# Kernel tuning notes

Measured on AMD Instinct MI355X. Metric: run time of the kernel, lower is better.

The kernel has to match this reference:

```python
import jax, jax.numpy as jnp
import numpy as np

N, F, C = 4096, 512, 512
NUM_HOPS, TOP_K, MASK_RATIO = 3, 8, 0.5
EPS = 1e-12


def setup_inputs() -> dict:
    key = jax.random.key(0)
    ks = jax.random.split(key, 8)
    return {
        "x": jax.random.normal(ks[0], (N, F), dtype=jnp.float32),
        "adj": jax.random.uniform(ks[1], (NUM_HOPS, N, N), dtype=jnp.float32),
        "rand_mask": jax.random.uniform(ks[2], (NUM_HOPS, N, N), dtype=jnp.float32),
        "W_in": jax.random.normal(ks[3], (F, C), dtype=jnp.float32) * 0.02,
        "b_in": jnp.zeros((C,), dtype=jnp.float32),
        "W_out": jax.random.normal(ks[4], (C, C), dtype=jnp.float32) * 0.02,
        "b_out": jnp.zeros((C,), dtype=jnp.float32),
        "alpha": jnp.ones((NUM_HOPS,), dtype=jnp.float32),
        "beta": jnp.full((1,), 0.5, dtype=jnp.float32),
    }


def reference(x, adj, rand_mask, W_in, b_in, W_out, b_out, alpha, beta):
    H_low = x @ W_in + b_in  # (N, C)
    # F.normalize(x, dim=-1) @ F.normalize(x.T, dim=0) == x_n @ x_n.T
    xn = x / jnp.maximum(jnp.linalg.norm(x, axis=-1, keepdims=True), EPS)
    sim = xn @ xn.T  # (N, N)
    a = jax.nn.softmax(alpha)
    rows = jnp.arange(N)[:, None]
    H_high = jnp.zeros((N, F), dtype=x.dtype)
    for k in range(NUM_HOPS):
        Akw = a[k] * adj[k] * sim  # (N, N)
        _, idx = jax.lax.top_k(Akw, TOP_K)  # (N, TOP_K)
        topk_mask = jnp.zeros_like(Akw).at[rows, idx].set(1.0)
        retain = (rand_mask[k] < MASK_RATIO).astype(Akw.dtype)
        final_mask = ((topk_mask + retain) > 0).astype(Akw.dtype)
        Hk = (Akw * final_mask) @ x  # (N, F)
        H_high = H_high + a[k] * Hk
    b = beta[0]
    H = jax.nn.relu(b * H_low + (1.0 - b) * H_high)
    # dropout in eval mode (identity)
    out = H @ W_out + b_out
    return jax.nn.log_softmax(out, axis=-1)
```

## Files before the change

kernel.cpp:

```cpp
#include <hip/hip_runtime.h>
#include <hip/hip_bf16.h>
#include <stdint.h>

#define NROW 4096
#define FDIM 512

typedef short bf16x8 __attribute__((ext_vector_type(8)));
typedef float f32x4 __attribute__((ext_vector_type(4)));
typedef float f4 __attribute__((ext_vector_type(4)));
typedef ushort u16x4 __attribute__((ext_vector_type(4)));

#define NEG_INF (-__builtin_inff())

__device__ inline ushort f2bf(float f) {
    union { float f; uint32_t u; } c{f};
    uint32_t u = c.u;
    uint32_t r = (u + 0x7FFF + ((u >> 16) & 1)) >> 16;
    return (ushort)r;
}
__device__ inline float bf2f(ushort h) {
    union { uint32_t u; float f; } c{((uint32_t)h) << 16};
    return c.f;
}
__device__ inline uint32_t cvt_pk_bf16(float lo, float hi) {
    uint32_t r;
    asm("v_cvt_pk_bf16_f32 %0, %1, %2" : "=v"(r) : "v"(lo), "v"(hi));
    return r;
}
__device__ inline float up0(uint32_t p) {
    union { uint32_t u; float f; } c{p << 16}; return c.f;
}
__device__ inline float up1(uint32_t p) {
    union { uint32_t u; float f; } c{p & 0xFFFF0000u}; return c.f;
}

__device__ inline float waveReduceMax(float v) {
    #pragma unroll
    for (int o = 32; o > 0; o >>= 1) v = fmaxf(v, __shfl_xor(v, o));
    return v;
}
__device__ inline float waveReduceSum(float v) {
    #pragma unroll
    for (int o = 32; o > 0; o >>= 1) v += __shfl_xor(v, o);
    return v;
}

__device__ inline void CE(float& a, float& b) {
    float mx = fmaxf(a, b);
    b = fminf(a, b);
    a = mx;
}
__device__ inline void sort8(float (&l)[8]) {
    CE(l[0],l[1]); CE(l[2],l[3]); CE(l[4],l[5]); CE(l[6],l[7]);
    CE(l[0],l[2]); CE(l[1],l[3]); CE(l[4],l[6]); CE(l[5],l[7]);
    CE(l[1],l[2]); CE(l[5],l[6]);
    CE(l[0],l[4]); CE(l[1],l[5]); CE(l[2],l[6]); CE(l[3],l[7]);
    CE(l[2],l[4]); CE(l[3],l[5]);
    CE(l[1],l[2]); CE(l[3],l[4]); CE(l[5],l[6]);
}
__device__ inline void mergeTop8(float (&a)[8], const float (&b)[8]) {
    float t[8];
    #pragma unroll
    for (int i = 0; i < 8; i++) t[i] = fmaxf(a[i], b[7 - i]);
    CE(t[0],t[4]); CE(t[1],t[5]); CE(t[2],t[6]); CE(t[3],t[7]);
    CE(t[0],t[2]); CE(t[1],t[3]); CE(t[4],t[6]); CE(t[5],t[7]);
    CE(t[0],t[1]); CE(t[2],t[3]); CE(t[4],t[5]); CE(t[6],t[7]);
    #pragma unroll
    for (int i = 0; i < 8; i++) a[i] = t[i];
}

#define GLL16(src, dst)                                                        \
    __builtin_amdgcn_global_load_lds(                                          \
        (const __attribute__((address_space(1))) void*)(src),                  \
        (__attribute__((address_space(3))) void*)(dst), 16, 0, 0)

__global__ __launch_bounds__(64) void coef_k(const float* __restrict__ alpha,
                                             const float* __restrict__ beta,
                                             float* __restrict__ coef) {
    if (threadIdx.x == 0) {
        float a0 = alpha[0], a1 = alpha[1], a2 = alpha[2];
        float m = fmaxf(a0, fmaxf(a1, a2));
        float e0 = expf(a0 - m), e1 = expf(a1 - m), e2 = expf(a2 - m);
        float s = e0 + e1 + e2;
        coef[0] = e0 / s; coef[1] = e1 / s; coef[2] = e2 / s;
        coef[3] = beta[0];
    }
}

__global__ __launch_bounds__(256) void prep_x(const float* __restrict__ x,
                                              ushort* __restrict__ xn,
                                              ushort* __restrict__ xb) {
    int row = blockIdx.x, tid = threadIdx.x;
    int lane = tid & 63, w = tid >> 6;
    const float* xr = x + (size_t)row * FDIM;
    float v0 = xr[tid], v1 = xr[tid + 256];
    float ss = v0 * v0 + v1 * v1;
    ss = waveReduceSum(ss);
    __shared__ float b4[4];
    if (lane == 0) b4[w] = ss;
    __syncthreads();
    float tot = b4[0] + b4[1] + b4[2] + b4[3];
    float inv = 1.f / fmaxf(sqrtf(tot), 1e-12f);
    size_t o = (size_t)row * FDIM + tid;
    xn[o] = f2bf(v0 * inv);  xn[o + 256] = f2bf(v1 * inv);
    xb[o] = f2bf(v0);        xb[o + 256] = f2bf(v1);
}

__global__ __launch_bounds__(256) void transpose_xb(const ushort* __restrict__ in,
                                                    ushort* __restrict__ out) {
    __shared__ ushort t[64][65];
    int lx = threadIdx.x & 63, ly = threadIdx.x >> 6;
    int c0 = blockIdx.x * 64, r0 = blockIdx.y * 64;
    #pragma unroll
    for (int i = 0; i < 16; i++)
        t[ly + 4 * i][lx] = in[(size_t)(r0 + ly + 4 * i) * FDIM + c0 + lx];
    __syncthreads();
    #pragma unroll
    for (int i = 0; i < 16; i++)
        out[(size_t)(c0 + ly + 4 * i) * NROW + r0 + lx] = t[lx][ly + 4 * i];
}

__global__ __launch_bounds__(256) void convT_w(const float* __restrict__ Wf,
                                               ushort* __restrict__ WT) {
    __shared__ ushort t[64][65];
    int lx = threadIdx.x & 63, ly = threadIdx.x >> 6;
    int c0 = blockIdx.x * 64, r0 = blockIdx.y * 64;
    #pragma unroll
    for (int i = 0; i < 16; i++)
        t[ly + 4 * i][lx] = f2bf(Wf[(size_t)(r0 + ly + 4 * i) * 512 + c0 + lx]);
    __syncthreads();
    #pragma unroll
    for (int i = 0; i < 16; i++)
        WT[(size_t)(c0 + ly + 4 * i) * 512 + r0 + lx] = t[lx][ly + 4 * i];
}

template <int EPI>
__global__ __launch_bounds__(256) void gemm_abT(
    const ushort* __restrict__ A, int lda,
    const ushort* __restrict__ B, int ldb,
    int Kdim, int ldc,
    float* __restrict__ Cf, ushort* __restrict__ Cb,
    const float* __restrict__ bias) {
    constexpr int BK = 64;
    constexpr int NT = 128 * BK;
    constexpr int CPR = BK / 8;
    constexpr int PASSES = (128 * CPR) / 256;
    __shared__ __align__(16) ushort smem[2 * NT];
    ushort* As = smem;
    ushort* Bs = smem + NT;

    if constexpr (EPI == 3) {
        A += (size_t)blockIdx.z * 1024;
        B += (size_t)blockIdx.z * 1024;
        Cf += (size_t)blockIdx.z * ((size_t)NROW * 512);
    }

    const int tid = threadIdx.x;
    const int lane = tid & 63, w = tid >> 6;
    const int wr = w >> 1, wc = w & 1;
    const int m0 = blockIdx.y * 128;
    const int n0 = blockIdx.x * 128;

    f32x4 acc[4][4];
    #pragma unroll
    for (int mi = 0; mi < 4; mi++)
        #pragma unroll
        for (int ni = 0; ni < 4; ni++)
            #pragma unroll
            for (int r = 0; r < 4; r++) acc[mi][ni][r] = 0.f;

    for (int k0 = 0; k0 < Kdim; k0 += BK) {
        #pragma unroll
        for (int p = 0; p < PASSES; ++p) {
            int chunk = p * 256 + tid;
            int row = chunk / CPR;
            int kc = chunk % CPR;
            const ushort* asrc = A + (size_t)(m0 + row) * lda + k0 + kc * 8;
            const ushort* bsrc = B + (size_t)(n0 + row) * ldb + k0 + kc * 8;
            ushort* abase = As + (size_t)(p * 256 + w * 64) * 8;
            ushort* bbase = Bs + (size_t)(p * 256 + w * 64) * 8;
            GLL16(asrc, abase);
            GLL16(bsrc, bbase);
        }
        __syncthreads();
        #pragma unroll
        for (int kf = 0; kf < BK / 32; ++kf) {
            const int ko = kf * 32 + (lane >> 4) * 8;
            bf16x8 av[4], bv[4];
            #pragma unroll
            for (int mi = 0; mi < 4; mi++)
                av[mi] = *(const bf16x8*)&As[(wr * 64 + mi * 16 + (lane & 15)) * BK + ko];
            #pragma unroll
            for (int ni = 0; ni < 4; ni++)
                bv[ni] = *(const bf16x8*)&Bs[(wc * 64 + ni * 16 + (lane & 15)) * BK + ko];
            #pragma unroll
            for (int mi = 0; mi < 4; mi++)
                #pragma unroll
                for (int ni = 0; ni < 4; ni++)
                    acc[mi][ni] = __builtin_amdgcn_mfma_f32_16x16x32_bf16(
                        av[mi], bv[ni], acc[mi][ni], 0, 0, 0);
        }
        __syncthreads();
    }

    #pragma unroll
    for (int mi = 0; mi < 4; mi++) {
        #pragma unroll
        for (int ni = 0; ni < 4; ni++) {
            int col = n0 + wc * 64 + ni * 16 + (lane & 15);
            #pragma unroll
            for (int r = 0; r < 4; r++) {
                int rowg = m0 + wr * 64 + mi * 16 + (lane >> 4) * 4 + r;
                size_t off = (size_t)rowg * ldc + col;
                float v = acc[mi][ni][r];
                if constexpr (EPI == 1) {
                    Cf[off] = v + bias[col];
                } else if constexpr (EPI == 3) {
                    Cf[off] = v;
                } else {
                    Cb[off] = f2bf(v);
                }
            }
        }
    }
}

__global__ __launch_bounds__(256) void topk_build_M(
    const ushort* __restrict__ simb, const float* __restrict__ adj,
    const float* __restrict__ rmask, const float* __restrict__ coef,
    ushort* __restrict__ Mout) {
    const int tid = threadIdx.x;
    const int lane = tid & 63;
    const int w = tid >> 6;
    const int row = blockIdx.x;
    __shared__ float wl[3][4][8];

    const int cbase = w * 1024 + lane * 4;

    const ushort* srow = simb + (size_t)row * NROW + cbase;
    uint2 svp[4];
    #pragma unroll
    for (int q = 0; q < 4; q++)
        svp[q] = *(const uint2*)(srow + q * 256);

    float macc[4][4];
    #pragma unroll
    for (int q = 0; q < 4; q++)
        #pragma unroll
        for (int c = 0; c < 4; c++) macc[q][c] = 0.f;

    for (int k = 0; k < 3; ++k) {
        const float* arow = adj + ((size_t)k * NROW + row) * NROW + cbase;
        const float* rrow = rmask + ((size_t)k * NROW + row) * NROW + cbase;

        f4 rv[4], a[4];
        #pragma unroll
        for (int q = 0; q < 4; q++) rv[q] = *(const f4*)(rrow + q * 256);
        #pragma unroll
        for (int q = 0; q < 4; q++) a[q] = *(const f4*)(arow + q * 256);

        uint32_t rbits = 0;
        #pragma unroll
        for (int q = 0; q < 4; q++) {
            rbits |= (rv[q].x < 0.5f ? 1u : 0u) << (q * 4 + 0);
            rbits |= (rv[q].y < 0.5f ? 1u : 0u) << (q * 4 + 1);
            rbits |= (rv[q].z < 0.5f ? 1u : 0u) << (q * 4 + 2);
            rbits |= (rv[q].w < 0.5f ? 1u : 0u) << (q * 4 + 3);
        }

        uint2 avp[4];
        #pragma unroll
        for (int q = 0; q < 4; q++) {
            avp[q].x = cvt_pk_bf16(a[q].x, a[q].y);
            avp[q].y = cvt_pk_bf16(a[q].z, a[q].w);
        }

        float lo8[8], hi8[8];
        #pragma unroll
        for (int qq = 0; qq < 2; qq++) {
            lo8[qq * 4 + 0] = up0(avp[qq].x) * up0(svp[qq].x);
            lo8[qq * 4 + 1] = up1(avp[qq].x) * up1(svp[qq].x);
            lo8[qq * 4 + 2] = up0(avp[qq].y) * up0(svp[qq].y);
            lo8[qq * 4 + 3] = up1(avp[qq].y) * up1(svp[qq].y);
        }
        #pragma unroll
        for (int qq = 0; qq < 2; qq++) {
            const int q = 2 + qq;
            hi8[qq * 4 + 0] = up0(avp[q].x) * up0(svp[q].x);
            hi8[qq * 4 + 1] = up1(avp[q].x) * up1(svp[q].x);
            hi8[qq * 4 + 2] = up0(avp[q].y) * up0(svp[q].y);
            hi8[qq * 4 + 3] = up1(avp[q].y) * up1(svp[q].y);
        }
        sort8(lo8);
        sort8(hi8);
        mergeTop8(lo8, hi8);

        #pragma unroll
        for (int lvl = 0; lvl < 6; lvl++) {
            float b[8];
            #pragma unroll
            for (int i = 0; i < 8; i++) b[i] = __shfl_xor(lo8[i], 1 << lvl);
            mergeTop8(lo8, b);
        }

        if (lane < 8) wl[k][w][lane] = lo8[lane];
        __syncthreads();
        #pragma unroll
        for (int ww = 0; ww < 4; ww++) {
            if (ww != w) {
                float b[8];
                #pragma unroll
                for (int i = 0; i < 8; i++) b[i] = wl[k][ww][i];
                mergeTop8(lo8, b);
            }
        }
        const float thr = lo8[7];

        const float ak = coef[k];
        const float aksq = ak * ak;
        #pragma unroll
        for (int q = 0; q < 4; q++) {
            float av0 = up0(avp[q].x), av1 = up1(avp[q].x);
            float av2 = up0(avp[q].y), av3 = up1(avp[q].y);
            float s0 = up0(svp[q].x), s1 = up1(svp[q].x);
            float s2 = up0(svp[q].y), s3 = up1(svp[q].y);
            bool m0 = ((rbits >> (q * 4 + 0)) & 1) || (av0 * s0 >= thr);
            bool m1 = ((rbits >> (q * 4 + 1)) & 1) || (av1 * s1 >= thr);
            bool m2 = ((rbits >> (q * 4 + 2)) & 1) || (av2 * s2 >= thr);
            bool m3 = ((rbits >> (q * 4 + 3)) & 1) || (av3 * s3 >= thr);
            macc[q][0] += m0 ? aksq * av0 : 0.f;
            macc[q][1] += m1 ? aksq * av1 : 0.f;
            macc[q][2] += m2 ? aksq * av2 : 0.f;
            macc[q][3] += m3 ? aksq * av3 : 0.f;
        }
    }

    ushort* mrow = Mout + (size_t)row * NROW + cbase;
    #pragma unroll
    for (int q = 0; q < 4; q++) {
        u16x4 o;
        o[0] = f2bf(up0(svp[q].x) * macc[q][0]);
        o[1] = f2bf(up1(svp[q].x) * macc[q][1]);
        o[2] = f2bf(up0(svp[q].y) * macc[q][2]);
        o[3] = f2bf(up1(svp[q].y) * macc[q][3]);
        *(u16x4*)(mrow + q * 256) = o;
    }
}

__global__ __launch_bounds__(256) void reduce_relu(
    const float* __restrict__ parts, const float* __restrict__ hlow,
    const float* __restrict__ coef, ushort* __restrict__ Hb) {
    const size_t i = (size_t)blockIdx.x * 256 + threadIdx.x;
    const f4* p4 = (const f4*)parts;
    f4 s = p4[i];
    #pragma unroll
    for (int z = 1; z < 4; z++) s += p4[(size_t)z * 524288 + i];
    f4 hl = ((const f4*)hlow)[i];
    float cb = coef[3];
    u16x4 o;
    #pragma unroll
    for (int c = 0; c < 4; c++) {
        float h = cb * hl[c] + (1.f - cb) * s[c];
        o[c] = f2bf(fmaxf(h, 0.f));
    }
    *((u16x4*)Hb + i) = o;
}

__global__ __launch_bounds__(256) void logsoftmax_k(const float* __restrict__ L,
                                                    float* __restrict__ out) {
    int row = blockIdx.x, tid = threadIdx.x;
    int lane = tid & 63, w = tid >> 6;
    const float* lr = L + (size_t)row * 512;
    float v0 = lr[tid], v1 = lr[tid + 256];
    __shared__ float bm[4], bs[4];
    float m = fmaxf(v0, v1);
    m = waveReduceMax(m);
    if (lane == 0) bm[w] = m;
    __syncthreads();
    float M = fmaxf(fmaxf(bm[0], bm[1]), fmaxf(bm[2], bm[3]));
    float s = expf(v0 - M) + expf(v1 - M);
    s = waveReduceSum(s);
    if (lane == 0) bs[w] = s;
    __syncthreads();
    float S = bs[0] + bs[1] + bs[2] + bs[3];
    float lse = M + logf(S);
    float* orow = out + (size_t)row * 512;
    orow[tid] = v0 - lse;
    orow[tid + 256] = v1 - lse;
}

extern "C" void kernel_launch(void* const* d_in, const int* in_sizes, int n_in,
                              void* d_out, int out_size, void* d_ws, size_t ws_size,
                              hipStream_t stream) {
    const float* x     = (const float*)d_in[0];
    const float* adj   = (const float*)d_in[1];
    const float* rmask = (const float*)d_in[2];
    const float* W_in  = (const float*)d_in[3];
    const float* b_in  = (const float*)d_in[4];
    const float* W_out = (const float*)d_in[5];
    const float* b_out = (const float*)d_in[6];
    const float* alpha = (const float*)d_in[7];
    const float* beta  = (const float*)d_in[8];
    float* out = (float*)d_out;

    const size_t MB = 1024 * 1024;
    char* wsb = (char*)d_ws;
    ushort* simb   = (ushort*)wsb;
    float*  parts  = (float*)wsb;
    float*  logits = (float*)wsb;
    ushort* Mb     = (ushort*)(wsb + 32 * MB);
    ushort* xn     = (ushort*)(wsb + 64 * MB);
    ushort* xb     = (ushort*)(wsb + 68 * MB);
    ushort* xbT    = (ushort*)(wsb + 72 * MB);
    ushort* WinT   = (ushort*)(wsb + 76 * MB);
    ushort* WoutT  = (ushort*)(wsb + 76 * MB + 512 * 1024);
    float*  Hlow   = (float*)(wsb + 77 * MB);
    ushort* Hb     = (ushort*)(wsb + 85 * MB);
    float*  coef   = (float*)(wsb + 89 * MB);

    coef_k<<<1, 64, 0, stream>>>(alpha, beta, coef);
    prep_x<<<NROW, 256, 0, stream>>>(x, xn, xb);
    transpose_xb<<<dim3(8, 64), 256, 0, stream>>>(xb, xbT);
    convT_w<<<dim3(8, 8), 256, 0, stream>>>(W_in, WinT);
    convT_w<<<dim3(8, 8), 256, 0, stream>>>(W_out, WoutT);

    gemm_abT<4><<<dim3(32, 32), 256, 0, stream>>>(
        xn, FDIM, xn, FDIM, FDIM, NROW, nullptr, simb, nullptr);

    topk_build_M<<<NROW, 256, 0, stream>>>(simb, adj, rmask, coef, Mb);

    gemm_abT<1><<<dim3(4, 32), 256, 0, stream>>>(
        xb, FDIM, WinT, FDIM, FDIM, 512, Hlow, nullptr, b_in);

    gemm_abT<3><<<dim3(4, 32, 4), 256, 0, stream>>>(
        Mb, NROW, xbT, NROW, 1024, 512, parts, nullptr, nullptr);

    reduce_relu<<<2048, 256, 0, stream>>>(parts, Hlow, coef, Hb);

    gemm_abT<1><<<dim3(4, 32), 256, 0, stream>>>(
        Hb, 512, WoutT, 512, 512, 512, logits, nullptr, b_out);

    logsoftmax_k<<<NROW, 256, 0, stream>>>(logits, out);
}
```

Baseline: 217.6 us.

## Assign one wavefront per row in top-k mask build, merge weight transpose launches

The top-k mask kernel now gives each row to a single wavefront instead of a whole block. This removes the shared-memory exchange and __syncthreads between waves. Each wave makes two passes: first it streams adj and sim to find the per-hop thresholds, then it re-reads adj, rand_mask and sim chunk by chunk to build M. The cost is a second read of adj from memory, or from cache if it still fits, in exchange for fewer syncs and lower register pressure. The two weight transpose kernels are also merged into a single launch.

```diff
diff --git a/kernel.cpp b/kernel.cpp
--- a/kernel.cpp
+++ b/kernel.cpp
@@ -120,8 +120,12 @@
         out[(size_t)(c0 + ly + 4 * i) * NROW + r0 + lx] = t[lx][ly + 4 * i];
 }
 
-__global__ __launch_bounds__(256) void convT_w(const float* __restrict__ Wf,
-                                               ushort* __restrict__ WT) {
+__global__ __launch_bounds__(256) void convT_w2(const float* __restrict__ W0,
+                                                ushort* __restrict__ T0,
+                                                const float* __restrict__ W1,
+                                                ushort* __restrict__ T1) {
+    const float* Wf = blockIdx.z ? W1 : W0;
+    ushort* WT = blockIdx.z ? T1 : T0;
     __shared__ ushort t[64][65];
     int lx = threadIdx.x & 63, ly = threadIdx.x >> 6;
     int c0 = blockIdx.x * 64, r0 = blockIdx.y * 64;
@@ -225,6 +229,68 @@
     }
 }
 
+__device__ __attribute__((always_inline)) inline void chunk_top8(
+    const f4 (&a)[4], const uint2 (&sp)[4], float (&t)[8]) {
+    float u[8];
+    #pragma unroll
+    for (int qq = 0; qq < 2; qq++) {
+        uint32_t p0 = cvt_pk_bf16(a[qq].x, a[qq].y);
+        uint32_t p1 = cvt_pk_bf16(a[qq].z, a[qq].w);
+        t[qq * 4 + 0] = up0(p0) * up0(sp[qq].x);
+        t[qq * 4 + 1] = up1(p0) * up1(sp[qq].x);
+        t[qq * 4 + 2] = up0(p1) * up0(sp[qq].y);
+        t[qq * 4 + 3] = up1(p1) * up1(sp[qq].y);
+    }
+    #pragma unroll
+    for (int qq = 0; qq < 2; qq++) {
+        const int q = 2 + qq;
+        uint32_t p0 = cvt_pk_bf16(a[q].x, a[q].y);
+        uint32_t p1 = cvt_pk_bf16(a[q].z, a[q].w);
+        u[qq * 4 + 0] = up0(p0) * up0(sp[q].x);
+        u[qq * 4 + 1] = up1(p0) * up1(sp[q].x);
+        u[qq * 4 + 2] = up0(p1) * up0(sp[q].y);
+        u[qq * 4 + 3] = up1(p1) * up1(sp[q].y);
+    }
+    sort8(t);
+    sort8(u);
+    mergeTop8(t, u);
+}
+
+template <int K>
+__device__ __attribute__((always_inline)) inline float hop_threshold(
+    const float* __restrict__ arow, const ushort* __restrict__ srow,
+    int loff) {
+    const size_t hopstride = (size_t)NROW * NROW;
+    float l[8];
+    #pragma unroll
+    for (int c = 0; c < 4; ++c) {
+        f4 a[4];
+        uint2 sp[4];
+        #pragma unroll
+        for (int q = 0; q < 4; q++)
+            a[q] = *(const f4*)(arow + K * hopstride + c * 1024 + q * 256 + loff);
+        #pragma unroll
+        for (int q = 0; q < 4; q++)
+            sp[q] = *(const uint2*)(srow + c * 1024 + q * 256 + loff);
+        float t[8];
+        chunk_top8(a, sp, t);
+        if (c == 0) {
+            #pragma unroll
+            for (int i = 0; i < 8; i++) l[i] = t[i];
+        } else {
+            mergeTop8(l, t);
+        }
+    }
+    #pragma unroll
+    for (int lvl = 0; lvl < 6; lvl++) {
+        float b[8];
+        #pragma unroll
+        for (int i = 0; i < 8; i++) b[i] = __shfl_xor(l[i], 1 << lvl);
+        mergeTop8(l, b);
+    }
+    return l[7];
+}
+
 __global__ __launch_bounds__(256) void topk_build_M(
     const ushort* __restrict__ simb, const float* __restrict__ adj,
     const float* __restrict__ rmask, const float* __restrict__ coef,
@@ -232,118 +298,74 @@
     const int tid = threadIdx.x;
     const int lane = tid & 63;
     const int w = tid >> 6;
-    const int row = blockIdx.x;
-    __shared__ float wl[3][4][8];
-
-    const int cbase = w * 1024 + lane * 4;
-
-    const ushort* srow = simb + (size_t)row * NROW + cbase;
-    uint2 svp[4];
-    #pragma unroll
-    for (int q = 0; q < 4; q++)
-        svp[q] = *(const uint2*)(srow + q * 256);
-
-    float macc[4][4];
-    #pragma unroll
-    for (int q = 0; q < 4; q++)
-        #pragma unroll
-        for (int c = 0; c < 4; c++) macc[q][c] = 0.f;
-
-    for (int k = 0; k < 3; ++k) {
-        const float* arow = adj + ((size_t)k * NROW + row) * NROW + cbase;
-        const float* rrow = rmask + ((size_t)k * NROW + row) * NROW + cbase;
-
-        f4 rv[4], a[4];
-        #pragma unroll
-        for (int q = 0; q < 4; q++) rv[q] = *(const f4*)(rrow + q * 256);
-        #pragma unroll
-        for (int q = 0; q < 4; q++) a[q] = *(const f4*)(arow + q * 256);
-
-        uint32_t rbits = 0;
+    const int row = blockIdx.x * 4 + w;
+    const int loff = lane * 4;
+    const size_t hopstride = (size_t)NROW * NROW;
+
+    const ushort* srow = simb + (size_t)row * NROW;
+    const float* arow = adj + (size_t)row * NROW;
+    const float* rrow = rmask + (size_t)row * NROW;
+
+    const float thr0 = hop_threshold<0>(arow, srow, loff);
+    const float thr1 = hop_threshold<1>(arow, srow, loff);
+    const float thr2 = hop_threshold<2>(arow, srow, loff);
+
+    const float c0 = coef[0], c1 = coef[1], c2 = coef[2];
+
+    #pragma unroll 1
+    for (int c = 0; c < 4; ++c) {
+        uint2 sp[4];
+        #pragma unroll
+        for (int q = 0; q < 4; q++)
+            sp[q] = *(const uint2*)(srow + c * 1024 + q * 256 + loff);
+
+        float macc[4][4];
+        #pragma unroll
+        for (int q = 0; q < 4; q++)
+            #pragma unroll
+            for (int e = 0; e < 4; e++) macc[q][e] = 0.f;
+
+        #pragma unroll
+        for (int k = 0; k < 3; ++k) {
+            const float ak = (k == 0) ? c0 : (k == 1) ? c1 : c2;
+            const float thr = (k == 0) ? thr0 : (k == 1) ? thr1 : thr2;
+            const float aksq = ak * ak;
+            f4 a[4], rv[4];
+            #pragma unroll
+            for (int q = 0; q < 4; q++)
+                rv[q] = *(const f4*)(rrow + k * hopstride + c * 1024 + q * 256 + loff);
+            #pragma unroll
+            for (int q = 0; q < 4; q++)
+                a[q] = *(const f4*)(arow + k * hopstride + c * 1024 + q * 256 + loff);
+            #pragma unroll
+            for (int q = 0; q < 4; q++) {
+                uint32_t p0 = cvt_pk_bf16(a[q].x, a[q].y);
+                uint32_t p1 = cvt_pk_bf16(a[q].z, a[q].w);
+                float av0 = up0(p0), av1 = up1(p0);
+                float av2 = up0(p1), av3 = up1(p1);
+                float s0 = up0(sp[q].x), s1 = up1(sp[q].x);
+                float s2 = up0(sp[q].y), s3 = up1(sp[q].y);
+                bool m0 = (rv[q].x < 0.5f) || (av0 * s0 >= thr);
+                bool m1 = (rv[q].y < 0.5f) || (av1 * s1 >= thr);
+                bool m2 = (rv[q].z < 0.5f) || (av2 * s2 >= thr);
+                bool m3 = (rv[q].w < 0.5f) || (av3 * s3 >= thr);
+                macc[q][0] += m0 ? aksq * av0 : 0.f;
+                macc[q][1] += m1 ? aksq * av1 : 0.f;
+                macc[q][2] += m2 ? aksq * av2 : 0.f;
+                macc[q][3] += m3 ? aksq * av3 : 0.f;
+            }
+        }
+
+        ushort* mrow = Mout + (size_t)row * NROW + c * 1024 + loff;
         #pragma unroll
         for (int q = 0; q < 4; q++) {
-            rbits |= (rv[q].x < 0.5f ? 1u : 0u) << (q * 4 + 0);
-            rbits |= (rv[q].y < 0.5f ? 1u : 0u) << (q * 4 + 1);
-            rbits |= (rv[q].z < 0.5f ? 1u : 0u) << (q * 4 + 2);
-            rbits |= (rv[q].w < 0.5f ? 1u : 0u) << (q * 4 + 3);
-        }
-
-        uint2 avp[4];
-        #pragma unroll
-        for (int q = 0; q < 4; q++) {
-            avp[q].x = cvt_pk_bf16(a[q].x, a[q].y);
-            avp[q].y = cvt_pk_bf16(a[q].z, a[q].w);
-        }
-
-        float lo8[8], hi8[8];
-        #pragma unroll
-        for (int qq = 0; qq < 2; qq++) {
-            lo8[qq * 4 + 0] = up0(avp[qq].x) * up0(svp[qq].x);
-            lo8[qq * 4 + 1] = up1(avp[qq].x) * up1(svp[qq].x);
-            lo8[qq * 4 + 2] = up0(avp[qq].y) * up0(svp[qq].y);
-            lo8[qq * 4 + 3] = up1(avp[qq].y) * up1(svp[qq].y);
-        }
-        #pragma unroll
-        for (int qq = 0; qq < 2; qq++) {
-            const int q = 2 + qq;
-            hi8[qq * 4 + 0] = up0(avp[q].x) * up0(svp[q].x);
-            hi8[qq * 4 + 1] = up1(avp[q].x) * up1(svp[q].x);
-            hi8[qq * 4 + 2] = up0(avp[q].y) * up0(svp[q].y);
-            hi8[qq * 4 + 3] = up1(avp[q].y) * up1(svp[q].y);
-        }
-        sort8(lo8);
-        sort8(hi8);
-        mergeTop8(lo8, hi8);
-
-        #pragma unroll
-        for (int lvl = 0; lvl < 6; lvl++) {
-            float b[8];
-            #pragma unroll
-            for (int i = 0; i < 8; i++) b[i] = __shfl_xor(lo8[i], 1 << lvl);
-            mergeTop8(lo8, b);
-        }
-
-        if (lane < 8) wl[k][w][lane] = lo8[lane];
-        __syncthreads();
-        #pragma unroll
-        for (int ww = 0; ww < 4; ww++) {
-            if (ww != w) {
-                float b[8];
-                #pragma unroll
-                for (int i = 0; i < 8; i++) b[i] = wl[k][ww][i];
-                mergeTop8(lo8, b);
-            }
-        }
-        const float thr = lo8[7];
-
-        const float ak = coef[k];
-        const float aksq = ak * ak;
-        #pragma unroll
-        for (int q = 0; q < 4; q++) {
-            float av0 = up0(avp[q].x), av1 = up1(avp[q].x);
-            float av2 = up0(avp[q].y), av3 = up1(avp[q].y);
-            float s0 = up0(svp[q].x), s1 = up1(svp[q].x);
-            float s2 = up0(svp[q].y), s3 = up1(svp[q].y);
-            bool m0 = ((rbits >> (q * 4 + 0)) & 1) || (av0 * s0 >= thr);
-            bool m1 = ((rbits >> (q * 4 + 1)) & 1) || (av1 * s1 >= thr);
-            bool m2 = ((rbits >> (q * 4 + 2)) & 1) || (av2 * s2 >= thr);
-            bool m3 = ((rbits >> (q * 4 + 3)) & 1) || (av3 * s3 >= thr);
-            macc[q][0] += m0 ? aksq * av0 : 0.f;
-            macc[q][1] += m1 ? aksq * av1 : 0.f;
-            macc[q][2] += m2 ? aksq * av2 : 0.f;
-            macc[q][3] += m3 ? aksq * av3 : 0.f;
-        }
-    }
-
-    ushort* mrow = Mout + (size_t)row * NROW + cbase;
-    #pragma unroll
-    for (int q = 0; q < 4; q++) {
-        u16x4 o;
-        o[0] = f2bf(up0(svp[q].x) * macc[q][0]);
-        o[1] = f2bf(up1(svp[q].x) * macc[q][1]);
-        o[2] = f2bf(up0(svp[q].y) * macc[q][2]);
-        o[3] = f2bf(up1(svp[q].y) * macc[q][3]);
-        *(u16x4*)(mrow + q * 256) = o;
+            u16x4 o;
+            o[0] = f2bf(up0(sp[q].x) * macc[q][0]);
+            o[1] = f2bf(up1(sp[q].x) * macc[q][1]);
+            o[2] = f2bf(up0(sp[q].y) * macc[q][2]);
+            o[3] = f2bf(up1(sp[q].y) * macc[q][3]);
+            *(u16x4*)(mrow + q * 256) = o;
+        }
     }
 }
 
@@ -421,13 +443,12 @@
     coef_k<<<1, 64, 0, stream>>>(alpha, beta, coef);
     prep_x<<<NROW, 256, 0, stream>>>(x, xn, xb);
     transpose_xb<<<dim3(8, 64), 256, 0, stream>>>(xb, xbT);
-    convT_w<<<dim3(8, 8), 256, 0, stream>>>(W_in, WinT);
-    convT_w<<<dim3(8, 8), 256, 0, stream>>>(W_out, WoutT);
+    convT_w2<<<dim3(8, 8, 2), 256, 0, stream>>>(W_in, WinT, W_out, WoutT);
 
     gemm_abT<4><<<dim3(32, 32), 256, 0, stream>>>(
         xn, FDIM, xn, FDIM, FDIM, NROW, nullptr, simb, nullptr);
 
-    topk_build_M<<<NROW, 256, 0, stream>>>(simb, adj, rmask, coef, Mb);
+    topk_build_M<<<NROW / 4, 256, 0, stream>>>(simb, adj, rmask, coef, Mb);
 
     gemm_abT<1><<<dim3(4, 32), 256, 0, stream>>>(
         xb, FDIM, WinT, FDIM, FDIM, 512, Hlow, nullptr, b_in);
```

Result: slower. 242.2 us (+11.3%).

## Exploit symmetry of similarity GEMM and fuse preprocessing kernels

Applied to the files above, without the earlier changes.

Replaces the full 32x32-tile xn·xnᵀ GEMM with a triangular launch of 528 tiles that computes only upper-triangle blocks and writes the transposed copy through shared memory. The separate prep, transpose and weight-conversion kernels are merged into one launch, and the x transpose now converts straight from the fp32 input. The top-k kernel's hop loop is kept rolled and gains a barrier. This roughly halves the similarity GEMM work and cuts launches, at the cost of strided transposed stores and a larger shared-memory tile.

```diff
diff --git a/kernel.cpp b/kernel.cpp
--- a/kernel.cpp
+++ b/kernel.cpp
@@ -17,10 +17,6 @@
     uint32_t u = c.u;
     uint32_t r = (u + 0x7FFF + ((u >> 16) & 1)) >> 16;
     return (ushort)r;
-}
-__device__ inline float bf2f(ushort h) {
-    union { uint32_t u; float f; } c{((uint32_t)h) << 16};
-    return c.f;
 }
 __device__ inline uint32_t cvt_pk_bf16(float lo, float hi) {
     uint32_t r;
@@ -87,51 +83,142 @@
     }
 }
 
-__global__ __launch_bounds__(256) void prep_x(const float* __restrict__ x,
-                                              ushort* __restrict__ xn,
-                                              ushort* __restrict__ xb) {
-    int row = blockIdx.x, tid = threadIdx.x;
-    int lane = tid & 63, w = tid >> 6;
-    const float* xr = x + (size_t)row * FDIM;
-    float v0 = xr[tid], v1 = xr[tid + 256];
-    float ss = v0 * v0 + v1 * v1;
-    ss = waveReduceSum(ss);
+__global__ __launch_bounds__(256) void prep_fused(
+    const float* __restrict__ x, ushort* __restrict__ xn,
+    ushort* __restrict__ xb, ushort* __restrict__ xbT,
+    const float* __restrict__ W_in, ushort* __restrict__ WinT,
+    const float* __restrict__ W_out, ushort* __restrict__ WoutT) {
+    const int b = blockIdx.x;
+    const int tid = threadIdx.x;
     __shared__ float b4[4];
-    if (lane == 0) b4[w] = ss;
-    __syncthreads();
-    float tot = b4[0] + b4[1] + b4[2] + b4[3];
-    float inv = 1.f / fmaxf(sqrtf(tot), 1e-12f);
-    size_t o = (size_t)row * FDIM + tid;
-    xn[o] = f2bf(v0 * inv);  xn[o + 256] = f2bf(v1 * inv);
-    xb[o] = f2bf(v0);        xb[o + 256] = f2bf(v1);
-}
-
-__global__ __launch_bounds__(256) void transpose_xb(const ushort* __restrict__ in,
-                                                    ushort* __restrict__ out) {
     __shared__ ushort t[64][65];
-    int lx = threadIdx.x & 63, ly = threadIdx.x >> 6;
-    int c0 = blockIdx.x * 64, r0 = blockIdx.y * 64;
-    #pragma unroll
-    for (int i = 0; i < 16; i++)
-        t[ly + 4 * i][lx] = in[(size_t)(r0 + ly + 4 * i) * FDIM + c0 + lx];
-    __syncthreads();
-    #pragma unroll
-    for (int i = 0; i < 16; i++)
-        out[(size_t)(c0 + ly + 4 * i) * NROW + r0 + lx] = t[lx][ly + 4 * i];
-}
-
-__global__ __launch_bounds__(256) void convT_w(const float* __restrict__ Wf,
-                                               ushort* __restrict__ WT) {
-    __shared__ ushort t[64][65];
-    int lx = threadIdx.x & 63, ly = threadIdx.x >> 6;
-    int c0 = blockIdx.x * 64, r0 = blockIdx.y * 64;
-    #pragma unroll
-    for (int i = 0; i < 16; i++)
-        t[ly + 4 * i][lx] = f2bf(Wf[(size_t)(r0 + ly + 4 * i) * 512 + c0 + lx]);
-    __syncthreads();
-    #pragma unroll
-    for (int i = 0; i < 16; i++)
-        WT[(size_t)(c0 + ly + 4 * i) * 512 + r0 + lx] = t[lx][ly + 4 * i];
+
+    if (b < 4096) {
+        const int row = b;
+        int lane = tid & 63, w = tid >> 6;
+        const float* xr = x + (size_t)row * FDIM;
+        float v0 = xr[tid], v1 = xr[tid + 256];
+        float ss = v0 * v0 + v1 * v1;
+        ss = waveReduceSum(ss);
+        if (lane == 0) b4[w] = ss;
+        __syncthreads();
+        float tot = b4[0] + b4[1] + b4[2] + b4[3];
+        float inv = 1.f / fmaxf(sqrtf(tot), 1e-12f);
+        size_t o = (size_t)row * FDIM + tid;
+        xn[o] = f2bf(v0 * inv);  xn[o + 256] = f2bf(v1 * inv);
+        xb[o] = f2bf(v0);        xb[o + 256] = f2bf(v1);
+    } else if (b < 4608) {
+        const int tb = b - 4096;
+        const int c0 = (tb & 7) * 64, r0 = (tb >> 3) * 64;
+        int lx = tid & 63, ly = tid >> 6;
+        #pragma unroll
+        for (int i = 0; i < 16; i++)
+            t[ly + 4 * i][lx] = f2bf(x[(size_t)(r0 + ly + 4 * i) * FDIM + c0 + lx]);
+        __syncthreads();
+        #pragma unroll
+        for (int i = 0; i < 16; i++)
+            xbT[(size_t)(c0 + ly + 4 * i) * NROW + r0 + lx] = t[lx][ly + 4 * i];
+    } else {
+        const int cb = b - 4608;
+        const float* Wf = (cb >> 6) ? W_out : W_in;
+        ushort* WT = (cb >> 6) ? WoutT : WinT;
+        const int idx = cb & 63;
+        const int c0 = (idx & 7) * 64, r0 = (idx >> 3) * 64;
+        int lx = tid & 63, ly = tid >> 6;
+        #pragma unroll
+        for (int i = 0; i < 16; i++)
+            t[ly + 4 * i][lx] = f2bf(Wf[(size_t)(r0 + ly + 4 * i) * 512 + c0 + lx]);
+        __syncthreads();
+        #pragma unroll
+        for (int i = 0; i < 16; i++)
+            WT[(size_t)(c0 + ly + 4 * i) * 512 + r0 + lx] = t[lx][ly + 4 * i];
+    }
+}
+
+__global__ __launch_bounds__(256) void gemm_sym(
+    const ushort* __restrict__ A, ushort* __restrict__ C) {
+    constexpr int BK = 64;
+    constexpr int NT = 128 * BK;
+    __shared__ __align__(16) ushort smem[128 * 130];
+    ushort* As = smem;
+    ushort* Bs = smem + NT;
+
+    int bi = 0, rem = blockIdx.x;
+    while (rem >= 32 - bi) { rem -= 32 - bi; bi++; }
+    const int bj = bi + rem;
+    const int m0 = bi * 128, n0 = bj * 128;
+
+    const int tid = threadIdx.x;
+    const int lane = tid & 63, w = tid >> 6;
+    const int wr = w >> 1, wc = w & 1;
+
+    f32x4 acc[4][4];
+    #pragma unroll
+    for (int mi = 0; mi < 4; mi++)
+        #pragma unroll
+        for (int ni = 0; ni < 4; ni++)
+            #pragma unroll
+            for (int r = 0; r < 4; r++) acc[mi][ni][r] = 0.f;
+
+    for (int k0 = 0; k0 < FDIM; k0 += BK) {
+        #pragma unroll
+        for (int p = 0; p < 4; ++p) {
+            int chunk = p * 256 + tid;
+            int row = chunk / 8;
+            int kc = chunk % 8;
+            GLL16(A + (size_t)(m0 + row) * FDIM + k0 + kc * 8,
+                  As + (size_t)(p * 256 + w * 64) * 8);
+            GLL16(A + (size_t)(n0 + row) * FDIM + k0 + kc * 8,
+                  Bs + (size_t)(p * 256 + w * 64) * 8);
+        }
+        __syncthreads();
+        #pragma unroll
+        for (int kf = 0; kf < BK / 32; ++kf) {
+            const int ko = kf * 32 + (lane >> 4) * 8;
+            bf16x8 av[4], bv[4];
+            #pragma unroll
+            for (int mi = 0; mi < 4; mi++)
+                av[mi] = *(const bf16x8*)&As[(wr * 64 + mi * 16 + (lane & 15)) * BK + ko];
+            #pragma unroll
+            for (int ni = 0; ni < 4; ni++)
+                bv[ni] = *(const bf16x8*)&Bs[(wc * 64 + ni * 16 + (lane & 15)) * BK + ko];
+            #pragma unroll
+            for (int mi = 0; mi < 4; mi++)
+                #pragma unroll
+                for (int ni = 0; ni < 4; ni++)
+                    acc[mi][ni] = __builtin_amdgcn_mfma_f32_16x16x32_bf16(
+                        av[mi], bv[ni], acc[mi][ni], 0, 0, 0);
+        }
+        __syncthreads();
+    }
+
+    #pragma unroll
+    for (int mi = 0; mi < 4; mi++) {
+        #pragma unroll
+        for (int ni = 0; ni < 4; ni++) {
+            int lcol = wc * 64 + ni * 16 + (lane & 15);
+            #pragma unroll
+            for (int r = 0; r < 4; r++) {
+                int lrow = wr * 64 + mi * 16 + (lane >> 4) * 4 + r;
+                ushort hv = f2bf(acc[mi][ni][r]);
+                C[(size_t)(m0 + lrow) * NROW + n0 + lcol] = hv;
+                smem[lrow * 130 + lcol] = hv;
+            }
+        }
+    }
+
+    if (bi != bj) {
+        __syncthreads();
+        const int wv = w;
+        #pragma unroll 4
+        for (int i = 0; i < 32; i++) {
+            int r2 = wv * 32 + i;
+            ushort a = smem[(lane * 2) * 130 + r2];
+            ushort bb = smem[(lane * 2 + 1) * 130 + r2];
+            uint32_t pk = (uint32_t)a | ((uint32_t)bb << 16);
+            *(uint32_t*)&C[(size_t)(n0 + r2) * NROW + m0 + lane * 2] = pk;
+        }
+    }
 }
 
 template <int EPI>
@@ -215,10 +302,8 @@
                 float v = acc[mi][ni][r];
                 if constexpr (EPI == 1) {
                     Cf[off] = v + bias[col];
-                } else if constexpr (EPI == 3) {
+                } else {
                     Cf[off] = v;
-                } else {
-                    Cb[off] = f2bf(v);
                 }
             }
         }
@@ -236,8 +321,12 @@
     __shared__ float wl[3][4][8];
 
     const int cbase = w * 1024 + lane * 4;
+    const size_t hopstride = (size_t)NROW * NROW;
 
     const ushort* srow = simb + (size_t)row * NROW + cbase;
+    const float* arow = adj + (size_t)row * NROW + cbase;
+    const float* rrow = rmask + (size_t)row * NROW + cbase;
+
     uint2 svp[4];
     #pragma unroll
     for (int q = 0; q < 4; q++)
@@ -249,15 +338,16 @@
         #pragma unroll
         for (int c = 0; c < 4; c++) macc[q][c] = 0.f;
 
+    #pragma unroll 1
     for (int k = 0; k < 3; ++k) {
-        const float* arow = adj + ((size_t)k * NROW + row) * NROW + cbase;
-        const float* rrow = rmask + ((size_t)k * NROW + row) * NROW + cbase;
+        const float* ar = arow + (size_t)k * hopstride;
+        const float* rr = rrow + (size_t)k * hopstride;
 
         f4 rv[4], a[4];
         #pragma unroll
-        for (int q = 0; q < 4; q++) rv[q] = *(const f4*)(rrow + q * 256);
-        #pragma unroll
-        for (int q = 0; q < 4; q++) a[q] = *(const f4*)(arow + q * 256);
+        for (int q = 0; q < 4; q++) rv[q] = *(const f4*)(rr + q * 256);
+        #pragma unroll
+        for (int q = 0; q < 4; q++) a[q] = *(const f4*)(ar + q * 256);
 
         uint32_t rbits = 0;
         #pragma unroll
@@ -333,6 +423,7 @@
             macc[q][2] += m2 ? aksq * av2 : 0.f;
             macc[q][3] += m3 ? aksq * av3 : 0.f;
         }
+        __syncthreads();
     }
 
     ushort* mrow = Mout + (size_t)row * NROW + cbase;
@@ -419,13 +510,11 @@
     float*  coef   = (float*)(wsb + 89 * MB);
 
     coef_k<<<1, 64, 0, stream>>>(alpha, beta, coef);
-    prep_x<<<NROW, 256, 0, stream>>>(x, xn, xb);
-    transpose_xb<<<dim3(8, 64), 256, 0, stream>>>(xb, xbT);
-    convT_w<<<dim3(8, 8), 256, 0, stream>>>(W_in, WinT);
-    convT_w<<<dim3(8, 8), 256, 0, stream>>>(W_out, WoutT);
-
-    gemm_abT<4><<<dim3(32, 32), 256, 0, stream>>>(
-        xn, FDIM, xn, FDIM, FDIM, NROW, nullptr, simb, nullptr);
+
+    prep_fused<<<4096 + 512 + 128, 256, 0, stream>>>(
+        x, xn, xb, xbT, W_in, WinT, W_out, WoutT);
+
+    gemm_sym<<<528, 256, 0, stream>>>(xn, simb);
 
     topk_build_M<<<NROW, 256, 0, stream>>>(simb, adj, rmask, coef, Mb);
 
```

New measurement: 213.5 us. No clear change (-1.9%).
